# Kernel tuning notes

Hardware: AMD Instinct MI355X
Metric: run time of the kernel (lower is better)

Reference implementation:

```python
import jax, jax.numpy as jnp
import numpy as np
from jax import lax

B, T, N_MELS = 8, 4096, 26
W_FRAMES = 32          # window_frames
CONV_CH, CONV_K = 64, 5
SE_MID = CONV_CH // 4  # se_ratio=4 on feature_dim=conv_channels
H1, H2 = 256, 128      # hidden_dims
SHORT_W, SHORT_H = 8, 128
OUT_CH = 2             # downbeat=True


def setup_inputs() -> dict:
    key = jax.random.key(0)
    ks = jax.random.split(key, 16)
    s = lambda *sh: 1.0 / np.sqrt(sh[0])
    return {
        "x": jax.random.normal(ks[0], (B, T, N_MELS), jnp.float32),
        # conv1d: kernel stored (K, in, out) for NWC/WIO conv
        "conv_w": jax.random.normal(ks[1], (CONV_K, N_MELS, CONV_CH), jnp.float32) * 0.1,
        "conv_b": jax.random.normal(ks[2], (CONV_CH,), jnp.float32) * 0.1,
        # SE on feature_dim=CONV_CH
        "se_w1": jax.random.normal(ks[3], (CONV_CH, SE_MID), jnp.float32) * s(CONV_CH),
        "se_b1": jnp.zeros((SE_MID,), jnp.float32),
        "se_w2": jax.random.normal(ks[4], (SE_MID, CONV_CH), jnp.float32) * s(SE_MID),
        "se_b2": jnp.zeros((CONV_CH,), jnp.float32),
        # long backbone: (W_FRAMES*CONV_CH) -> H1 -> H2
        "w1": jax.random.normal(ks[5], (W_FRAMES * CONV_CH, H1), jnp.float32) * s(W_FRAMES * CONV_CH),
        "b1": jnp.zeros((H1,), jnp.float32),
        "w2": jax.random.normal(ks[6], (H1, H2), jnp.float32) * s(H1),
        "b2": jnp.zeros((H2,), jnp.float32),
        # short backbone: (SHORT_W*CONV_CH) -> SHORT_H
        "sw": jax.random.normal(ks[7], (SHORT_W * CONV_CH, SHORT_H), jnp.float32) * s(SHORT_W * CONV_CH),
        "sb": jnp.zeros((SHORT_H,), jnp.float32),
        # output head: (H2 + SHORT_H) -> OUT_CH
        "wo": jax.random.normal(ks[8], (H2 + SHORT_H, OUT_CH), jnp.float32) * s(H2 + SHORT_H),
        "bo": jnp.zeros((OUT_CH,), jnp.float32),
    }


def reference(x, conv_w, conv_b, se_w1, se_b1, se_w2, se_b2,
              w1, b1, w2, b2, sw, sb, wo, bo):
    batch, time, _ = x.shape
    # 1) causal conv1d over full sequence (left-pad K-1), then ReLU
    xp = jnp.pad(x, ((0, 0), (CONV_K - 1, 0), (0, 0)))
    xc = lax.conv_general_dilated(xp, conv_w, window_strides=(1,),
                                  padding='VALID',
                                  dimension_numbers=('NWC', 'WIO', 'NWC'))
    xc = jax.nn.relu(xc + conv_b)                      # (B, T, F=CONV_CH)
    # 2) causal sliding-window unfold: windows[b,t,w,:] = padded[b, t+w, :]
    x_pad = jnp.pad(xc, ((0, 0), (W_FRAMES - 1, 0), (0, 0)))
    idx = jnp.arange(time)[:, None] + jnp.arange(W_FRAMES)[None, :]
    windows = x_pad[:, idx, :]                          # (B, T, W, F)
    # 3) SE channel attention (pool over window dim)
    s = windows.mean(axis=2)                            # (B, T, F)
    a = jax.nn.sigmoid(jax.nn.relu(s @ se_w1 + se_b1) @ se_w2 + se_b2)
    windows = windows * a[:, :, None, :]
    # 4) long backbone (dropout = identity in eval)
    flat_long = windows.reshape(batch, time, W_FRAMES * CONV_CH)
    h = jax.nn.relu(flat_long @ w1 + b1)
    h = jax.nn.relu(h @ w2 + b2)                        # (B, T, H2)
    # short path: last SHORT_W frames of the same SE-processed window
    flat_short = windows[:, :, -SHORT_W:, :].reshape(batch, time, SHORT_W * CONV_CH)
    h_short = jax.nn.relu(flat_short @ sw + sb)         # (B, T, SHORT_H)
    h = jnp.concatenate([h, h_short], axis=-1)
    # 5) output head
    return jax.nn.sigmoid(h @ wo + bo)                  # (B, T, OUT_CH)
```

## Files before the change

### kernel.cpp

```cpp
#include <hip/hip_runtime.h>

typedef _Float16 half_t;
typedef __attribute__((ext_vector_type(8))) _Float16 h8;
typedef __attribute__((ext_vector_type(2))) _Float16 h2v;
typedef __attribute__((ext_vector_type(4))) float f4;
typedef __attribute__((ext_vector_type(2))) float f2v;

__device__ __forceinline__ half_t to_h(float v) {
    v = fminf(fmaxf(v, -60000.f), 60000.f);
    return (half_t)v;
}

__global__ void pack_k(const float* __restrict__ w1, const float* __restrict__ w2,
                       const float* __restrict__ sw, const float* __restrict__ cw,
                       half_t* __restrict__ wsH) {
    int i = blockIdx.x * 256 + threadIdx.x;
    if (i < 65536) {
        int L = i & 63, nt = (i >> 6) & 15, kk = i >> 10;
        int k0 = kk * 32 + ((L >> 4) << 3), n = (nt << 4) + (L & 15);
        h8 v;
#pragma unroll
        for (int j = 0; j < 8; j++) v[j] = to_h(w1[(k0 + j) * 256 + n]);
        *(h8*)(wsH + ((((kk * 16 + nt) * 64 + L)) << 3)) = v;
    } else if (i < 69632) {
        int o = i - 65536;
        int L = o & 63, nt = (o >> 6) & 7, kk = o >> 9;
        int k0 = kk * 32 + ((L >> 4) << 3), n = (nt << 4) + (L & 15);
        h8 v;
#pragma unroll
        for (int j = 0; j < 8; j++) v[j] = to_h(w2[(k0 + j) * 128 + n]);
        *(h8*)(wsH + 524288 + ((((kk * 8 + nt) * 64 + L)) << 3)) = v;
    } else if (i < 77824) {
        int o = i - 69632;
        int L = o & 63, nt = (o >> 6) & 7, kk = o >> 9;
        int k0 = kk * 32 + ((L >> 4) << 3), n = (nt << 4) + (L & 15);
        h8 v;
#pragma unroll
        for (int j = 0; j < 8; j++) v[j] = to_h(sw[(k0 + j) * 128 + n]);
        *(h8*)(wsH + 557056 + ((((kk * 8 + nt) * 64 + L)) << 3)) = v;
    } else if (i < 86144) {
        int o = i - 77824;
        int c = o & 63, rest = o >> 6;
        int k = rest / 26, ci = rest - k * 26;
        int ip = ci >> 1, r = ci & 1;
        wsH[622592 + ((k * 13 + ip) * 64 + c) * 2 + r] = to_h(cw[o]);
    }
}

#define XCS 72
#define XLS 32
#define ALS 72
#define Y1S 264
#define SLS 68
#define HLS 20

#define MFMA16(a, b, c) __builtin_amdgcn_mfma_f32_16x16x32_f16(a, b, c, 0, 0, 0)

__global__ __launch_bounds__(512, 4) void beat_main(
    const float* __restrict__ x,
    const float* __restrict__ conv_b,
    const float* __restrict__ se_w1, const float* __restrict__ se_b1,
    const float* __restrict__ se_w2, const float* __restrict__ se_b2,
    const float* __restrict__ b1, const float* __restrict__ b2,
    const float* __restrict__ sb,
    const float* __restrict__ wo, const float* __restrict__ bo,
    const half_t* __restrict__ w1p, const half_t* __restrict__ w2p,
    const half_t* __restrict__ swp, const half_t* __restrict__ cwp,
    float* __restrict__ out) {

    __shared__ __align__(16) char smem[58752];
    half_t* xcL = (half_t*)smem;
    half_t* aL  = (half_t*)(smem + 13696);
    char*   U   = smem + 22912;
    half_t* xLh = (half_t*)U;
    float*  sLf = (float*)U;
    float*  hidL= (float*)(U + 17408);
    half_t* y1L = (half_t*)U;
    float*  woL = (float*)(smem + 56704);

    const int tid = threadIdx.x;
    const int bi = blockIdx.x;
    const int b = bi >> 6;
    const int t0 = (bi & 63) << 6;
    const int lane = tid & 63, wv = tid >> 6;
    const int quad = lane >> 4, rl = lane & 15;

    if (tid < 256) ((f2v*)woL)[tid] = ((const f2v*)wo)[tid];
    for (int idx = tid; idx < 99 * 13; idx += 512) {
        int fi = idx / 13, ip = idx - fi * 13;
        int tx = t0 - 35 + fi;
        h2v v;
        if (tx >= 0) {
            const float* xp = x + ((size_t)(b * 4096 + tx)) * 26 + 2 * ip;
            v[0] = to_h(xp[0]); v[1] = to_h(xp[1]);
        } else { v[0] = (_Float16)0.f; v[1] = (_Float16)0.f; }
        *(h2v*)(xLh + fi * XLS + 2 * ip) = v;
    }
    __syncthreads();

    {
        int c = tid & 63, f0 = tid >> 6;
        h2v cwr[65];
        const h2v* cwg = (const h2v*)cwp;
#pragma unroll
        for (int p = 0; p < 65; p++) cwr[p] = cwg[p * 64 + c];
        float bias = conv_b[c];
        for (int f = f0; f < 95; f += 8) {
            int t = t0 - 31 + f;
            float r0 = 0.f;
            if (t >= 0) {
                h2v accp; accp[0] = (_Float16)0.f; accp[1] = (_Float16)0.f;
#pragma unroll
                for (int k = 0; k < 5; k++) {
                    const half_t* rp = xLh + (f + k) * XLS;
                    h8 xa = *(const h8*)rp;
                    h8 xb = *(const h8*)(rp + 8);
                    h8 xc2 = *(const h8*)(rp + 16);
                    h2v xd = *(const h2v*)(rp + 24);
                    h2v xs[13];
#pragma unroll
                    for (int ii = 0; ii < 4; ii++) {
                        xs[ii][0]     = xa[2 * ii];  xs[ii][1]     = xa[2 * ii + 1];
                        xs[4 + ii][0] = xb[2 * ii];  xs[4 + ii][1] = xb[2 * ii + 1];
                        xs[8 + ii][0] = xc2[2 * ii]; xs[8 + ii][1] = xc2[2 * ii + 1];
                    }
                    xs[12] = xd;
#pragma unroll
                    for (int ip = 0; ip < 13; ip++)
                        accp += xs[ip] * cwr[k * 13 + ip];
                }
                r0 = fmaxf((float)accp[0] + (float)accp[1] + bias, 0.f);
            }
            xcL[f * XCS + c] = to_h(r0);
        }
    }
    __syncthreads();

    {
        int m = tid >> 3, cg = tid & 7;
        const half_t* base = xcL + m * XCS + cg * 8;
        f4 a0, a1;
#pragma unroll
        for (int r = 0; r < 4; r++) { a0[r] = 0.f; a1[r] = 0.f; }
#pragma unroll
        for (int w = 0; w < 32; w++) {
            h8 v = *(const h8*)(base + w * XCS);
#pragma unroll
            for (int q = 0; q < 4; q++) { a0[q] += (float)v[q]; a1[q] += (float)v[4 + q]; }
        }
        float* sp = sLf + m * SLS + cg * 8;
        *(f4*)sp       = a0 * (1.f / 32.f);
        *(f4*)(sp + 4) = a1 * (1.f / 32.f);
    }
    __syncthreads();

    {
        int m = tid >> 3, hh = (tid & 7) * 2;
        float acc0 = se_b1[hh], acc1 = se_b1[hh + 1];
        for (int c = 0; c < 64; c++) {
            float sv = sLf[m * SLS + c];
            f2v wq = *(const f2v*)(se_w1 + c * 16 + hh);
            acc0 += sv * wq[0]; acc1 += sv * wq[1];
        }
        hidL[m * HLS + hh] = fmaxf(acc0, 0.f);
        hidL[m * HLS + hh + 1] = fmaxf(acc1, 0.f);
    }
    __syncthreads();

    {
        int m = tid >> 3, c0 = (tid & 7) * 8;
        float av[8];
#pragma unroll
        for (int j = 0; j < 8; j++) av[j] = se_b2[c0 + j];
        for (int h = 0; h < 16; h++) {
            float hv = hidL[m * HLS + h];
            const f4* wv4 = (const f4*)(se_w2 + h * 64 + c0);
            f4 wq0 = wv4[0], wq1 = wv4[1];
#pragma unroll
            for (int j = 0; j < 4; j++) { av[j] += hv * wq0[j]; av[4 + j] += hv * wq1[j]; }
        }
#pragma unroll
        for (int j = 0; j < 8; j++) {
            float zz = fminf(fmaxf(av[j], -30.f), 30.f);
            float s = 1.f / (1.f + __expf(-zz));
            aL[m * ALS + c0 + j] = to_h(s);
        }
    }
    __syncthreads();

    h8 avr[4][2];
#pragma unroll
    for (int mt = 0; mt < 4; mt++)
#pragma unroll
        for (int p = 0; p < 2; p++)
            avr[mt][p] = *(const h8*)(aL + (mt * 16 + rl) * ALS + p * 32 + quad * 8);

    {
        f4 acc[4][2];
#pragma unroll
        for (int mt = 0; mt < 4; mt++)
#pragma unroll
            for (int i = 0; i < 2; i++)
#pragma unroll
                for (int r = 0; r < 4; r++) acc[mt][i][r] = 0.f;
        const h8* w1v = (const h8*)w1p;
        const int fb = wv * 2;
        h8 bA[2], bB[2], bC[2], bD[2];
#pragma unroll
        for (int i = 0; i < 2; i++) bA[i] = w1v[(fb + i) * 64 + lane];
#pragma unroll
        for (int i = 0; i < 2; i++) bB[i] = w1v[(16 + fb + i) * 64 + lane];
#pragma unroll 2
        for (int kk = 0; kk < 64; kk += 2) {
            const int k2 = (kk + 2) & 63, k3 = (kk + 3) & 63;
#pragma unroll
            for (int i = 0; i < 2; i++) bC[i] = w1v[(k2 * 16 + fb + i) * 64 + lane];
#pragma unroll
            for (int i = 0; i < 2; i++) bD[i] = w1v[(k3 * 16 + fb + i) * 64 + lane];
            const int wf = kk >> 1;
            {
                const int c0 = quad * 8;
#pragma unroll
                for (int mt = 0; mt < 4; mt++) {
                    int m = mt * 16 + rl;
                    h8 xv = *(const h8*)(xcL + (m + wf) * XCS + c0);
                    h8 af = xv * avr[mt][0];
                    acc[mt][0] = MFMA16(af, bA[0], acc[mt][0]);
                    acc[mt][1] = MFMA16(af, bA[1], acc[mt][1]);
                }
            }
            {
                const int c0 = 32 + quad * 8;
#pragma unroll
                for (int mt = 0; mt < 4; mt++) {
                    int m = mt * 16 + rl;
                    h8 xv = *(const h8*)(xcL + (m + wf) * XCS + c0);
                    h8 af = xv * avr[mt][1];
                    acc[mt][0] = MFMA16(af, bB[0], acc[mt][0]);
                    acc[mt][1] = MFMA16(af, bB[1], acc[mt][1]);
                }
            }
#pragma unroll
            for (int i = 0; i < 2; i++) { bA[i] = bC[i]; bB[i] = bD[i]; }
        }
#pragma unroll
        for (int i = 0; i < 2; i++) {
            int n = wv * 32 + i * 16 + rl;
            float bb = b1[n];
#pragma unroll
            for (int mt = 0; mt < 4; mt++)
#pragma unroll
                for (int r = 0; r < 4; r++) {
                    int m = mt * 16 + quad * 4 + r;
                    y1L[m * Y1S + n] = to_h(fmaxf(acc[mt][i][r] + bb, 0.f));
                }
        }
    }
    __syncthreads();

    f4 acc2[4];
#pragma unroll
    for (int mt = 0; mt < 4; mt++)
#pragma unroll
        for (int r = 0; r < 4; r++) acc2[mt][r] = 0.f;
    {
        const h8* w2v = (const h8*)w2p;
        h8 cf = w2v[wv * 64 + lane];
#pragma unroll 2
        for (int kk = 0; kk < 8; kk++) {
            int kn = (kk + 1) & 7;
            h8 nf = w2v[(kn * 8 + wv) * 64 + lane];
#pragma unroll
            for (int mt = 0; mt < 4; mt++) {
                h8 av = *(const h8*)(y1L + (mt * 16 + rl) * Y1S + kk * 32 + quad * 8);
                acc2[mt] = MFMA16(av, cf, acc2[mt]);
            }
            cf = nf;
        }
    }

    f4 accS[4];
#pragma unroll
    for (int mt = 0; mt < 4; mt++)
#pragma unroll
        for (int r = 0; r < 4; r++) accS[mt][r] = 0.f;
    {
        const h8* swv = (const h8*)swp;
        h8 cf = swv[wv * 64 + lane];
#pragma unroll 2
        for (int kk = 0; kk < 16; kk++) {
            int kn = (kk + 1) & 15;
            h8 nf = swv[(kn * 8 + wv) * 64 + lane];
            const int wf = 24 + (kk >> 1);
            const int c0 = ((kk & 1) << 5) + quad * 8;
#pragma unroll
            for (int mt = 0; mt < 4; mt++) {
                int m = mt * 16 + rl;
                h8 xv = *(const h8*)(xcL + (m + wf) * XCS + c0);
                h8 af = xv * avr[mt][kk & 1];
                accS[mt] = MFMA16(af, cf, accS[mt]);
            }
            cf = nf;
        }
    }
    __syncthreads();

    {
        int n = wv * 16 + rl;
        float bb2 = b2[n], bbs = sb[n];
#pragma unroll
        for (int mt = 0; mt < 4; mt++)
#pragma unroll
            for (int r = 0; r < 4; r++) {
                int m = mt * 16 + quad * 4 + r;
                y1L[m * Y1S + n]       = to_h(fmaxf(acc2[mt][r] + bb2, 0.f));
                y1L[m * Y1S + 128 + n] = to_h(fmaxf(accS[mt][r] + bbs, 0.f));
            }
    }
    __syncthreads();

    if (tid < 128) {
        int m = tid >> 1, o = tid & 1;
        float z = bo[o];
        const half_t* hrow = y1L + m * Y1S;
        for (int nb = 0; nb < 32; nb++) {
            h8 hv = *(const h8*)(hrow + nb * 8);
#pragma unroll
            for (int q = 0; q < 8; q++)
                z += (float)hv[q] * woL[(nb * 8 + q) * 2 + o];
        }
        z = fminf(fmaxf(z, -30.f), 30.f);
        float sg = 1.f / (1.f + __expf(-z));
        out[((size_t)(b * 4096 + t0 + m)) * 2 + o] = sg;
    }
}

extern "C" void kernel_launch(void* const* d_in, const int* in_sizes, int n_in,
                              void* d_out, int out_size, void* d_ws, size_t ws_size,
                              hipStream_t stream) {
    const float* x      = (const float*)d_in[0];
    const float* conv_w = (const float*)d_in[1];
    const float* conv_b = (const float*)d_in[2];
    const float* se_w1  = (const float*)d_in[3];
    const float* se_b1  = (const float*)d_in[4];
    const float* se_w2  = (const float*)d_in[5];
    const float* se_b2  = (const float*)d_in[6];
    const float* w1     = (const float*)d_in[7];
    const float* b1     = (const float*)d_in[8];
    const float* w2     = (const float*)d_in[9];
    const float* b2     = (const float*)d_in[10];
    const float* sw     = (const float*)d_in[11];
    const float* sb     = (const float*)d_in[12];
    const float* wo     = (const float*)d_in[13];
    const float* bo     = (const float*)d_in[14];
    half_t* wsH = (half_t*)d_ws;

    hipLaunchKernelGGL(pack_k, dim3(337), dim3(256), 0, stream, w1, w2, sw, conv_w, wsH);
    hipLaunchKernelGGL(beat_main, dim3(512), dim3(512), 0, stream,
                       x, conv_b, se_w1, se_b1, se_w2, se_b2, b1, b2, sb, wo, bo,
                       wsH, wsH + 524288, wsH + 557056, wsH + 622592,
                       (float*)d_out);
}
```

Measured before the change: 144.2 us.

## Compute causal conv1d with MFMA instead of scalar packed-half FMAs

Replaces the per-thread scalar conv loop, which held 65 packed weight registers per thread, with 16x16x32 f16 MFMA tiles. The conv weights are repacked into the MFMA B-operand layout with input channels zero-padded from 26 to 32. The padding columns of the staged input tile are zeroed so the extra K lanes contribute nothing. This is meant to cut VALU work and register pressure in the conv stage, at the cost of roughly 23% wasted K lanes and a layout-dependent repack.

```diff
diff --git a/kernel.cpp b/kernel.cpp
--- a/kernel.cpp
+++ b/kernel.cpp
@@ -38,12 +38,17 @@
 #pragma unroll
         for (int j = 0; j < 8; j++) v[j] = to_h(sw[(k0 + j) * 128 + n]);
         *(h8*)(wsH + 557056 + ((((kk * 8 + nt) * 64 + L)) << 3)) = v;
-    } else if (i < 86144) {
+    } else if (i < 79104) {
         int o = i - 77824;
-        int c = o & 63, rest = o >> 6;
-        int k = rest / 26, ci = rest - k * 26;
-        int ip = ci >> 1, r = ci & 1;
-        wsH[622592 + ((k * 13 + ip) * 64 + c) * 2 + r] = to_h(cw[o]);
+        int L = o & 63, nt = (o >> 6) & 3, k5 = o >> 8;
+        int n = nt * 16 + (L & 15);
+        h8 v;
+#pragma unroll
+        for (int j = 0; j < 8; j++) {
+            int kin = ((L >> 4) << 3) + j;
+            v[j] = (kin < 26) ? to_h(cw[(k5 * 26 + kin) * 64 + n]) : (half_t)0.f;
+        }
+        *(h8*)(wsH + 622592 + ((size_t)o << 3)) = v;
     }
 }
 
@@ -65,7 +70,7 @@
     const float* __restrict__ sb,
     const float* __restrict__ wo, const float* __restrict__ bo,
     const half_t* __restrict__ w1p, const half_t* __restrict__ w2p,
-    const half_t* __restrict__ swp, const half_t* __restrict__ cwp,
+    const half_t* __restrict__ swp, const half_t* __restrict__ cwB,
     float* __restrict__ out) {
 
     __shared__ __align__(16) char smem[58752];
@@ -96,42 +101,39 @@
         } else { v[0] = (_Float16)0.f; v[1] = (_Float16)0.f; }
         *(h2v*)(xLh + fi * XLS + 2 * ip) = v;
     }
-    __syncthreads();
-
-    {
-        int c = tid & 63, f0 = tid >> 6;
-        h2v cwr[65];
-        const h2v* cwg = (const h2v*)cwp;
-#pragma unroll
-        for (int p = 0; p < 65; p++) cwr[p] = cwg[p * 64 + c];
-        float bias = conv_b[c];
-        for (int f = f0; f < 95; f += 8) {
-            int t = t0 - 31 + f;
-            float r0 = 0.f;
-            if (t >= 0) {
-                h2v accp; accp[0] = (_Float16)0.f; accp[1] = (_Float16)0.f;
-#pragma unroll
-                for (int k = 0; k < 5; k++) {
-                    const half_t* rp = xLh + (f + k) * XLS;
-                    h8 xa = *(const h8*)rp;
-                    h8 xb = *(const h8*)(rp + 8);
-                    h8 xc2 = *(const h8*)(rp + 16);
-                    h2v xd = *(const h2v*)(rp + 24);
-                    h2v xs[13];
-#pragma unroll
-                    for (int ii = 0; ii < 4; ii++) {
-                        xs[ii][0]     = xa[2 * ii];  xs[ii][1]     = xa[2 * ii + 1];
-                        xs[4 + ii][0] = xb[2 * ii];  xs[4 + ii][1] = xb[2 * ii + 1];
-                        xs[8 + ii][0] = xc2[2 * ii]; xs[8 + ii][1] = xc2[2 * ii + 1];
-                    }
-                    xs[12] = xd;
-#pragma unroll
-                    for (int ip = 0; ip < 13; ip++)
-                        accp += xs[ip] * cwr[k * 13 + ip];
+    for (int idx = tid; idx < 99 * 3; idx += 512) {
+        int fi = idx / 3, p = idx - fi * 3;
+        h2v z; z[0] = (_Float16)0.f; z[1] = (_Float16)0.f;
+        *(h2v*)(xLh + fi * XLS + 26 + 2 * p) = z;
+    }
+    __syncthreads();
+
+    {
+        const h8* cwv = (const h8*)cwB;
+#pragma unroll
+        for (int s = 0; s < 3; s++) {
+            int u = wv + 8 * s;
+            int rb = u >> 2, nt = u & 3;
+            f4 acc;
+#pragma unroll
+            for (int r = 0; r < 4; r++) acc[r] = 0.f;
+#pragma unroll
+            for (int k5 = 0; k5 < 5; k5++) {
+                h8 xv = *(const h8*)(xLh + (rb * 16 + rl + k5) * XLS + quad * 8);
+                h8 bf = cwv[(k5 * 4 + nt) * 64 + lane];
+                acc = MFMA16(xv, bf, acc);
+            }
+            int n = nt * 16 + rl;
+            float bias = conv_b[n];
+#pragma unroll
+            for (int r = 0; r < 4; r++) {
+                int m = rb * 16 + quad * 4 + r;
+                if (m < 95) {
+                    int t = t0 - 31 + m;
+                    float v = (t >= 0) ? fmaxf(acc[r] + bias, 0.f) : 0.f;
+                    xcL[m * XCS + n] = to_h(v);
                 }
-                r0 = fmaxf((float)accp[0] + (float)accp[1] + bias, 0.f);
-            }
-            xcL[f * XCS + c] = to_h(r0);
+            }
         }
     }
     __syncthreads();
```

Result: no change. 142.8 us (-1.0%).
